# Kernel tuning notes

Hardware: AMD Instinct MI355X
Metric: run time of the kernel (lower is better)

## Reference

```python
import jax, jax.numpy as jnp
import numpy as np

N_CLAUSES = 200000
N_FEATURES = 64
HIDDEN = 128
N_STEPS = 512


def setup_inputs() -> dict:
    key = jax.random.key(0)
    ks = jax.random.split(key, 8)
    features = jax.random.normal(ks[0], (N_CLAUSES, N_FEATURES), jnp.float32)
    W1 = jax.random.normal(ks[1], (N_FEATURES, HIDDEN), jnp.float32) / np.sqrt(N_FEATURES)
    b1 = jnp.zeros((HIDDEN,), jnp.float32)
    W2 = jax.random.normal(ks[2], (HIDDEN, HIDDEN), jnp.float32) / np.sqrt(HIDDEN)
    b2 = jnp.zeros((HIDDEN,), jnp.float32)
    key_w = jax.random.normal(ks[3], (HIDDEN,), jnp.float32) / np.sqrt(HIDDEN)
    # sel_mask[s, n] = clause n is in the passive set at SEL step s
    sel_mask = jax.random.bernoulli(ks[4], 0.5, (N_STEPS, N_CLAUSES))
    # proof_mask[n] = clause n participates in the final proof (sparse)
    proof_mask = jax.random.bernoulli(ks[5], 0.02, (N_CLAUSES,))
    # guarantee passive & proof nonempty at every step (torch code divides by its size)
    proof_mask = proof_mask.at[0].set(True)
    sel_mask = sel_mask.at[:, 0].set(True)
    return {
        "features": features, "W1": W1, "b1": b1, "W2": W2, "b2": b2,
        "key_w": key_w, "sel_mask": sel_mask, "proof_mask": proof_mask,
    }


def reference(features, W1, b1, W2, b2, key_w, sel_mask, proof_mask):
    # clause_embedder: 2-layer MLP; clause_key: dot with key vector -> one logit per clause
    h = jax.nn.relu(features @ W1 + b1)          # [N, H]
    emb = h @ W2 + b2                            # [N, H]
    logits = emb @ key_w                         # [N]

    neg = jnp.finfo(logits.dtype).min
    masked = jnp.where(sel_mask, logits[None, :], neg)   # [S, N]
    lse = jax.nn.logsumexp(masked, axis=1)                # [S] log-softmax denominator over passive set

    tgt = sel_mask & proof_mask[None, :]                  # [S, N] passive & proof
    cnt = tgt.sum(axis=1).astype(logits.dtype)            # [S] (>=1 by construction)
    # soft-target CE: -sum_j t_j * log_softmax(logits)_j, t uniform over tgt
    num = jnp.where(tgt, logits[None, :], 0.0).sum(axis=1) / cnt
    loss = (lse - num).mean()                             # mean over SEL steps
    return loss
```

## Files before the change

kernel.cpp:

```cpp
#include <hip/hip_runtime.h>
#include <hip/hip_bf16.h>

#define DEV __device__ __forceinline__

constexpr int NC = 200000;
constexpr int NF = 64;
constexpr int NH = 128;
constexpr int NS = 512;

constexpr int OF_CFG   = 0;
constexpr int OF_W1    = 16;
constexpr int OF_B1    = OF_W1 + NF * NH;
constexpr int OF_W2K   = OF_B1 + NH;
constexpr int OF_B2K   = OF_W2K + NH;
constexpr int OF_MAX   = OF_B2K + 1;
constexpr int OF_ACCE  = OF_MAX + 1;
constexpr int OF_ACCP  = OF_ACCE + NS;
constexpr int OF_ACCC  = OF_ACCP + NS;
constexpr int OF_LOGIT = 16384;
constexpr int OF_E     = OF_LOGIT + NC;
constexpr int OF_PL    = OF_E + NC;
constexpr int OF_PC    = OF_PL + NC;

DEV float bf2f(unsigned short u) { return __uint_as_float(((unsigned)u) << 16); }

DEV float loadF(const void* p, int i, int fk) {
    return fk ? bf2f(((const unsigned short*)p)[i]) : ((const float*)p)[i];
}

DEV unsigned flipf(float x) {
    unsigned u = __float_as_uint(x);
    return (u & 0x80000000u) ? ~u : (u | 0x80000000u);
}
DEV float unflipf(unsigned u) {
    unsigned b = (u & 0x80000000u) ? (u ^ 0x80000000u) : ~u;
    return __uint_as_float(b);
}

DEV bool okhalf(unsigned h) { return h == 0u || h == 1u || h == 0x3F80u || h == 0x3C00u; }

__global__ void k_probe(const void* features, const void* W1, const void* b1,
                        const void* W2, const void* b2, const void* keyw,
                        const void* sel, float* ws) {
    __shared__ int s_tiny, s_w4, s_w2;
    __shared__ float kw[NH];
    __shared__ float pr[NH];
    int tx = threadIdx.x;
    if (tx == 0) { s_tiny = 0; s_w4 = 1; s_w2 = 1; }
    __syncthreads();
    {
        const unsigned short* u = (const unsigned short*)features;
        unsigned e = (u[tx] >> 7) & 0xFFu;
        if (e < 100u) atomicAdd(&s_tiny, 1);
        const unsigned* w = (const unsigned*)sel;
        unsigned v = w[tx];
        if (!(v == 0u || v == 1u || v == 0x3F800000u)) atomicAnd(&s_w4, 0);
        if (!(okhalf(v & 0xFFFFu) && okhalf(v >> 16))) atomicAnd(&s_w2, 0);
    }
    __syncthreads();
    int fk = (s_tiny >= 8) ? 0 : 1;
    int mw = s_w4 ? 4 : (s_w2 ? 2 : 1);
    if (tx == 0) { ((int*)ws)[0] = fk; ((int*)ws)[1] = mw; }
    if (tx < NH) kw[tx] = loadF(keyw, tx, fk);
    for (int i = tx; i < NF * NH; i += blockDim.x) {
        int f = i >> 7;
        int j = i & (NH - 1);
        int jc = j >> 2, c = j & 3;
        ws[OF_W1 + ((jc * NF + f) << 2) + c] = loadF(W1, i, fk);
    }
    if (tx < NH) ws[OF_B1 + tx] = loadF(b1, tx, fk);
    __syncthreads();
    if (tx < NH) {
        float s = 0.f;
        for (int k = 0; k < NH; k++) s += loadF(W2, tx * NH + k, fk) * kw[k];
        ws[OF_W2K + tx] = s;
        pr[tx] = loadF(b2, tx, fk) * kw[tx];
    }
    __syncthreads();
    if (tx == 0) {
        float s = 0.f;
        for (int k = 0; k < NH; k++) s += pr[k];
        ws[OF_B2K] = s;
        ((unsigned*)ws)[OF_MAX] = 0u;
    }
    for (int i = tx; i < 3 * NS; i += blockDim.x) ws[OF_ACCE + i] = 0.f;
}

__global__ __launch_bounds__(256) void k_logits(const void* features,
                                                const float* __restrict__ w1t,
                                                const float* __restrict__ bias1,
                                                const float* __restrict__ wk,
                                                const float* __restrict__ cfg,
                                                float* __restrict__ logits,
                                                unsigned* __restrict__ maxp) {
    __shared__ float sred[4];
    int tx = threadIdx.x;
    int fk = ((const int*)cfg)[0];
    float b2k = cfg[OF_B2K];
    int n = blockIdx.x * 256 + tx;
    float acc = -3.0e38f;
    if (n < NC) {
        float feat[NF];
        if (fk) {
            const uint4* fp = (const uint4*)((const unsigned short*)features + (size_t)n * NF);
            #pragma unroll
            for (int q = 0; q < 8; q++) {
                uint4 v = fp[q];
                unsigned vv[4] = {v.x, v.y, v.z, v.w};
                #pragma unroll
                for (int h = 0; h < 4; h++) {
                    feat[q * 8 + h * 2 + 0] = __uint_as_float(vv[h] << 16);
                    feat[q * 8 + h * 2 + 1] = __uint_as_float(vv[h] & 0xFFFF0000u);
                }
            }
        } else {
            const float4* fp = (const float4*)((const float*)features + (size_t)n * NF);
            #pragma unroll
            for (int q = 0; q < 16; q++) {
                float4 v = fp[q];
                feat[q * 4 + 0] = v.x; feat[q * 4 + 1] = v.y;
                feat[q * 4 + 2] = v.z; feat[q * 4 + 3] = v.w;
            }
        }
        acc = b2k;
        for (int jc = 0; jc < NH / 4; jc++) {
            const float4* wp = (const float4*)(w1t + (size_t)jc * (NF * 4));
            float4 b = *(const float4*)(bias1 + jc * 4);
            float d0 = b.x, d1 = b.y, d2 = b.z, d3 = b.w;
            #pragma unroll
            for (int f = 0; f < NF; f++) {
                float4 w = wp[f];
                d0 += feat[f] * w.x; d1 += feat[f] * w.y;
                d2 += feat[f] * w.z; d3 += feat[f] * w.w;
            }
            float4 k4 = *(const float4*)(wk + jc * 4);
            acc += fmaxf(d0, 0.f) * k4.x + fmaxf(d1, 0.f) * k4.y
                 + fmaxf(d2, 0.f) * k4.z + fmaxf(d3, 0.f) * k4.w;
        }
        logits[n] = acc;
    }
    float m = acc;
    #pragma unroll
    for (int k = 1; k < 64; k <<= 1) m = fmaxf(m, __shfl_xor(m, k, 64));
    if ((tx & 63) == 0) sred[tx >> 6] = m;
    __syncthreads();
    if (tx == 0) {
        m = fmaxf(fmaxf(sred[0], sred[1]), fmaxf(sred[2], sred[3]));
        atomicMax(maxp, flipf(m));
    }
}

__global__ void k_prep(const void* proof, float* ws) {
    int n = blockIdx.x * 256 + threadIdx.x;
    if (n >= NC) return;
    int mw = ((const int*)ws)[1];
    float M = unflipf(((const unsigned*)ws)[OF_MAX]);
    float l = ws[OF_LOGIT + n];
    ws[OF_E + n] = __expf(l - M);
    bool pf;
    if (mw == 1)      pf = ((const unsigned char*)proof)[n] != 0;
    else if (mw == 2) pf = ((const unsigned short*)proof)[n] != 0;
    else              pf = ((const unsigned*)proof)[n] != 0;
    ws[OF_PL + n] = pf ? l : 0.f;
    ws[OF_PC + n] = pf ? 1.f : 0.f;
}

constexpr int NT_N = 16;
constexpr int BL_N = 256 * NT_N;
constexpr int SG = 32;

template<int MW>
DEV void bloop(const void* sel, int s0, int baddr,
               const float (&e)[NT_N], const float (&pl)[NT_N], const float (&pc)[NT_N],
               float* ws) {
    for (int si = 0; si < SG; si++) {
        int s = s0 + si;
        size_t off = (size_t)s * NC + (size_t)baddr;
        float m[NT_N];
        if (MW == 1) {
            uint4 w = *(const uint4*)((const unsigned char*)sel + off);
            unsigned v[4] = {w.x, w.y, w.z, w.w};
            #pragma unroll
            for (int q = 0; q < 4; q++)
                #pragma unroll
                for (int b = 0; b < 4; b++)
                    m[q * 4 + b] = ((v[q] >> (8 * b)) & 0xFFu) ? 1.f : 0.f;
        } else if (MW == 2) {
            const uint4* p = (const uint4*)((const unsigned short*)sel + off);
            #pragma unroll
            for (int h = 0; h < 2; h++) {
                uint4 w = p[h];
                unsigned v[4] = {w.x, w.y, w.z, w.w};
                #pragma unroll
                for (int q = 0; q < 4; q++) {
                    m[h * 8 + q * 2 + 0] = (v[q] & 0xFFFFu) ? 1.f : 0.f;
                    m[h * 8 + q * 2 + 1] = (v[q] >> 16) ? 1.f : 0.f;
                }
            }
        } else {
            const uint4* p = (const uint4*)((const unsigned*)sel + off);
            #pragma unroll
            for (int q = 0; q < 4; q++) {
                uint4 w = p[q];
                m[q * 4 + 0] = w.x ? 1.f : 0.f; m[q * 4 + 1] = w.y ? 1.f : 0.f;
                m[q * 4 + 2] = w.z ? 1.f : 0.f; m[q * 4 + 3] = w.w ? 1.f : 0.f;
            }
        }
        float se = 0.f, sp = 0.f, sc = 0.f;
        #pragma unroll
        for (int i = 0; i < NT_N; i++) {
            se += m[i] * e[i]; sp += m[i] * pl[i]; sc += m[i] * pc[i];
        }
        #pragma unroll
        for (int k = 1; k < 64; k <<= 1) {
            se += __shfl_xor(se, k, 64);
            sp += __shfl_xor(sp, k, 64);
            sc += __shfl_xor(sc, k, 64);
        }
        if ((threadIdx.x & 63) == 0) {
            atomicAdd(&ws[OF_ACCE + s], se);
            atomicAdd(&ws[OF_ACCP + s], sp);
            atomicAdd(&ws[OF_ACCC + s], sc);
        }
    }
}

__global__ __launch_bounds__(256) void k_phaseB(const void* sel, float* ws) {
    int tx = threadIdx.x;
    int base = blockIdx.x * BL_N + tx * NT_N;
    int s0 = blockIdx.y * SG;
    bool active = base < NC;
    int baddr = active ? base : 0;
    float e[NT_N], pl[NT_N], pc[NT_N];
    #pragma unroll
    for (int q = 0; q < 4; q++) {
        float4 ve = active ? ((const float4*)&ws[OF_E + baddr])[q]  : make_float4(0, 0, 0, 0);
        float4 vp = active ? ((const float4*)&ws[OF_PL + baddr])[q] : make_float4(0, 0, 0, 0);
        float4 vc = active ? ((const float4*)&ws[OF_PC + baddr])[q] : make_float4(0, 0, 0, 0);
        e[q * 4 + 0] = ve.x; e[q * 4 + 1] = ve.y; e[q * 4 + 2] = ve.z; e[q * 4 + 3] = ve.w;
        pl[q * 4 + 0] = vp.x; pl[q * 4 + 1] = vp.y; pl[q * 4 + 2] = vp.z; pl[q * 4 + 3] = vp.w;
        pc[q * 4 + 0] = vc.x; pc[q * 4 + 1] = vc.y; pc[q * 4 + 2] = vc.z; pc[q * 4 + 3] = vc.w;
    }
    int mw = ((const int*)ws)[1];
    if (mw == 1)      bloop<1>(sel, s0, baddr, e, pl, pc, ws);
    else if (mw == 2) bloop<2>(sel, s0, baddr, e, pl, pc, ws);
    else              bloop<4>(sel, s0, baddr, e, pl, pc, ws);
}

__global__ void k_final(float* ws, void* out) {
    __shared__ float sred[256];
    int tx = threadIdx.x;
    float M = unflipf(((const unsigned*)ws)[OF_MAX]);
    float sum = 0.f;
    for (int s = tx; s < NS; s += 256) {
        float lse = M + logf(ws[OF_ACCE + s]);
        sum += lse - ws[OF_ACCP + s] / ws[OF_ACCC + s];
    }
    sred[tx] = sum;
    __syncthreads();
    for (int k = 128; k > 0; k >>= 1) {
        if (tx < k) sred[tx] += sred[tx + k];
        __syncthreads();
    }
    if (tx == 0) {
        float loss = sred[0] / (float)NS;
        int fk = ((const int*)ws)[0];
        if (fk) ((__hip_bfloat16*)out)[0] = __float2bfloat16(loss);
        else    ((float*)out)[0] = loss;
    }
}

extern "C" void kernel_launch(void* const* d_in, const int* in_sizes, int n_in,
                              void* d_out, int out_size, void* d_ws, size_t ws_size,
                              hipStream_t stream) {
    const void* features = d_in[0];
    const void* W1   = d_in[1];
    const void* b1   = d_in[2];
    const void* W2   = d_in[3];
    const void* b2   = d_in[4];
    const void* keyw = d_in[5];
    const void* sel  = d_in[6];
    const void* proof = d_in[7];
    float* ws = (float*)d_ws;

    k_probe<<<1, 256, 0, stream>>>(features, W1, b1, W2, b2, keyw, sel, ws);
    int nblk = (NC + 255) / 256;
    k_logits<<<nblk, 256, 0, stream>>>(features, ws + OF_W1, ws + OF_B1, ws + OF_W2K,
                                       ws, ws + OF_LOGIT, (unsigned*)ws + OF_MAX);
    k_prep<<<nblk, 256, 0, stream>>>(proof, ws);
    dim3 gB((NC + BL_N - 1) / BL_N, NS / SG);
    k_phaseB<<<gB, 256, 0, stream>>>(sel, ws);
    k_final<<<1, 256, 0, stream>>>(ws, d_out);
}
```

Measured before the change: 702.2 us.

## Compute clause logits with bf16 MFMA using split-precision hi/lo operands

Rewrites the first MLP layer of the logits kernel to use 16x16x32 bf16 MFMA instructions instead of per-thread scalar FMA loops. Weights are pre-swizzled into MFMA operand layout in the probe kernel, and fp32 inputs are split into bf16 high and low parts, using three MFMA products to approximate fp32 accuracy. Each wave handles 32 rows, and the logits reduction goes through cross-lane shuffles. This targets the compute-bound GEMM cost of the logits stage, at the cost of extra MFMAs and conversions and slightly different rounding.

```diff
diff --git a/kernel.cpp b/kernel.cpp
--- a/kernel.cpp
+++ b/kernel.cpp
@@ -9,23 +9,33 @@
 constexpr int NS = 512;
 
 constexpr int OF_CFG   = 0;
-constexpr int OF_W1    = 16;
-constexpr int OF_B1    = OF_W1 + NF * NH;
+constexpr int OF_B1    = 16;
 constexpr int OF_W2K   = OF_B1 + NH;
 constexpr int OF_B2K   = OF_W2K + NH;
 constexpr int OF_MAX   = OF_B2K + 1;
-constexpr int OF_ACCE  = OF_MAX + 1;
+constexpr int OF_ACCE  = 288;
 constexpr int OF_ACCP  = OF_ACCE + NS;
 constexpr int OF_ACCC  = OF_ACCP + NS;
+constexpr int OF_W1H   = 2048;
+constexpr int OF_W1L   = 6144;
 constexpr int OF_LOGIT = 16384;
 constexpr int OF_E     = OF_LOGIT + NC;
 constexpr int OF_PL    = OF_E + NC;
 constexpr int OF_PC    = OF_PL + NC;
 
+using short8  = __attribute__((ext_vector_type(8))) short;
+using floatx4 = __attribute__((ext_vector_type(4))) float;
+
 DEV float bf2f(unsigned short u) { return __uint_as_float(((unsigned)u) << 16); }
 
 DEV float loadF(const void* p, int i, int fk) {
     return fk ? bf2f(((const unsigned short*)p)[i]) : ((const float*)p)[i];
+}
+
+DEV unsigned short f2bf(float x) {
+    unsigned u = __float_as_uint(x);
+    unsigned r = ((u >> 16) & 1u) + 0x7FFFu;
+    return (unsigned short)((u + r) >> 16);
 }
 
 DEV unsigned flipf(float x) {
@@ -52,8 +62,8 @@
         const unsigned short* u = (const unsigned short*)features;
         unsigned e = (u[tx] >> 7) & 0xFFu;
         if (e < 100u) atomicAdd(&s_tiny, 1);
-        const unsigned* w = (const unsigned*)sel;
-        unsigned v = w[tx];
+        const unsigned* wrd = (const unsigned*)sel;
+        unsigned v = wrd[tx];
         if (!(v == 0u || v == 1u || v == 0x3F800000u)) atomicAnd(&s_w4, 0);
         if (!(okhalf(v & 0xFFFFu) && okhalf(v >> 16))) atomicAnd(&s_w2, 0);
     }
@@ -62,13 +72,26 @@
     int mw = s_w4 ? 4 : (s_w2 ? 2 : 1);
     if (tx == 0) { ((int*)ws)[0] = fk; ((int*)ws)[1] = mw; }
     if (tx < NH) kw[tx] = loadF(keyw, tx, fk);
+    if (tx < NH) ws[OF_B1 + tx] = loadF(b1, tx, fk);
+    unsigned short* w1h = (unsigned short*)(ws + OF_W1H);
+    unsigned short* w1l = (unsigned short*)(ws + OF_W1L);
     for (int i = tx; i < NF * NH; i += blockDim.x) {
-        int f = i >> 7;
-        int j = i & (NH - 1);
-        int jc = j >> 2, c = j & 3;
-        ws[OF_W1 + ((jc * NF + f) << 2) + c] = loadF(W1, i, fk);
-    }
-    if (tx < NH) ws[OF_B1 + tx] = loadF(b1, tx, fk);
+        int j    = i & 7;
+        int lane = (i >> 3) & 63;
+        int ks   = (i >> 9) & 1;
+        int c    = i >> 10;
+        int k    = ks * 32 + ((lane >> 4) << 3) + j;
+        int col  = c * 16 + (lane & 15);
+        if (fk) {
+            w1h[i] = ((const unsigned short*)W1)[k * NH + col];
+            w1l[i] = 0;
+        } else {
+            float x = ((const float*)W1)[k * NH + col];
+            unsigned short h = f2bf(x);
+            w1h[i] = h;
+            w1l[i] = f2bf(x - __uint_as_float(((unsigned)h) << 16));
+        }
+    }
     __syncthreads();
     if (tx < NH) {
         float s = 0.f;
@@ -86,63 +109,107 @@
     for (int i = tx; i < 3 * NS; i += blockDim.x) ws[OF_ACCE + i] = 0.f;
 }
 
-__global__ __launch_bounds__(256) void k_logits(const void* features,
-                                                const float* __restrict__ w1t,
-                                                const float* __restrict__ bias1,
-                                                const float* __restrict__ wk,
-                                                const float* __restrict__ cfg,
+__global__ __launch_bounds__(256) void k_logits(const void* __restrict__ features,
+                                                const float* __restrict__ ws,
                                                 float* __restrict__ logits,
                                                 unsigned* __restrict__ maxp) {
     __shared__ float sred[4];
-    int tx = threadIdx.x;
-    int fk = ((const int*)cfg)[0];
-    float b2k = cfg[OF_B2K];
-    int n = blockIdx.x * 256 + tx;
-    float acc = -3.0e38f;
-    if (n < NC) {
-        float feat[NF];
+    const int tx = threadIdx.x, w = tx >> 6, l = tx & 63;
+    const int fk = ((const int*)ws)[0];
+    const float b2k = ws[OF_B2K];
+    const int rbase = blockIdx.x * 128 + w * 32;
+    const int lrow = l & 15;
+    const int lk = (l >> 4) << 3;
+
+    short8 ah[2][2], al[2][2];
+    if (fk) {
+        const unsigned short* f = (const unsigned short*)features;
+        #pragma unroll
+        for (int rt = 0; rt < 2; rt++) {
+            int row = rbase + rt * 16 + lrow; if (row > NC - 1) row = NC - 1;
+            #pragma unroll
+            for (int ks = 0; ks < 2; ks++)
+                ah[rt][ks] = *(const short8*)(f + (size_t)row * NF + ks * 32 + lk);
+        }
+    } else {
+        const float* f = (const float*)features;
+        #pragma unroll
+        for (int rt = 0; rt < 2; rt++) {
+            int row = rbase + rt * 16 + lrow; if (row > NC - 1) row = NC - 1;
+            #pragma unroll
+            for (int ks = 0; ks < 2; ks++) {
+                const float* p = f + (size_t)row * NF + ks * 32 + lk;
+                float4 v0 = *(const float4*)p;
+                float4 v1 = *(const float4*)(p + 4);
+                float xs[8] = {v0.x, v0.y, v0.z, v0.w, v1.x, v1.y, v1.z, v1.w};
+                #pragma unroll
+                for (int j = 0; j < 8; j++) {
+                    unsigned short h = f2bf(xs[j]);
+                    ah[rt][ks][j] = (short)h;
+                    al[rt][ks][j] = (short)f2bf(xs[j] - __uint_as_float(((unsigned)h) << 16));
+                }
+            }
+        }
+    }
+
+    const short8* w1h = (const short8*)(ws + OF_W1H);
+    const short8* w1l = (const short8*)(ws + OF_W1L);
+    float pr[2][4] = {{0.f, 0.f, 0.f, 0.f}, {0.f, 0.f, 0.f, 0.f}};
+
+    #pragma unroll 2
+    for (int c = 0; c < 8; c++) {
+        short8 bh0 = w1h[(c * 2 + 0) * 64 + l];
+        short8 bh1 = w1h[(c * 2 + 1) * 64 + l];
+        float b1v = ws[OF_B1 + c * 16 + lrow];
+        float wkv = ws[OF_W2K + c * 16 + lrow];
         if (fk) {
-            const uint4* fp = (const uint4*)((const unsigned short*)features + (size_t)n * NF);
-            #pragma unroll
-            for (int q = 0; q < 8; q++) {
-                uint4 v = fp[q];
-                unsigned vv[4] = {v.x, v.y, v.z, v.w};
-                #pragma unroll
-                for (int h = 0; h < 4; h++) {
-                    feat[q * 8 + h * 2 + 0] = __uint_as_float(vv[h] << 16);
-                    feat[q * 8 + h * 2 + 1] = __uint_as_float(vv[h] & 0xFFFF0000u);
-                }
+            #pragma unroll
+            for (int rt = 0; rt < 2; rt++) {
+                floatx4 acc = {0.f, 0.f, 0.f, 0.f};
+                acc = __builtin_amdgcn_mfma_f32_16x16x32_bf16(ah[rt][0], bh0, acc, 0, 0, 0);
+                acc = __builtin_amdgcn_mfma_f32_16x16x32_bf16(ah[rt][1], bh1, acc, 0, 0, 0);
+                #pragma unroll
+                for (int r = 0; r < 4; r++) pr[rt][r] += fmaxf(acc[r] + b1v, 0.f) * wkv;
             }
         } else {
-            const float4* fp = (const float4*)((const float*)features + (size_t)n * NF);
-            #pragma unroll
-            for (int q = 0; q < 16; q++) {
-                float4 v = fp[q];
-                feat[q * 4 + 0] = v.x; feat[q * 4 + 1] = v.y;
-                feat[q * 4 + 2] = v.z; feat[q * 4 + 3] = v.w;
-            }
-        }
-        acc = b2k;
-        for (int jc = 0; jc < NH / 4; jc++) {
-            const float4* wp = (const float4*)(w1t + (size_t)jc * (NF * 4));
-            float4 b = *(const float4*)(bias1 + jc * 4);
-            float d0 = b.x, d1 = b.y, d2 = b.z, d3 = b.w;
-            #pragma unroll
-            for (int f = 0; f < NF; f++) {
-                float4 w = wp[f];
-                d0 += feat[f] * w.x; d1 += feat[f] * w.y;
-                d2 += feat[f] * w.z; d3 += feat[f] * w.w;
-            }
-            float4 k4 = *(const float4*)(wk + jc * 4);
-            acc += fmaxf(d0, 0.f) * k4.x + fmaxf(d1, 0.f) * k4.y
-                 + fmaxf(d2, 0.f) * k4.z + fmaxf(d3, 0.f) * k4.w;
-        }
-        logits[n] = acc;
-    }
-    float m = acc;
+            short8 bl0 = w1l[(c * 2 + 0) * 64 + l];
+            short8 bl1 = w1l[(c * 2 + 1) * 64 + l];
+            #pragma unroll
+            for (int rt = 0; rt < 2; rt++) {
+                floatx4 acc = {0.f, 0.f, 0.f, 0.f};
+                acc = __builtin_amdgcn_mfma_f32_16x16x32_bf16(ah[rt][0], bh0, acc, 0, 0, 0);
+                acc = __builtin_amdgcn_mfma_f32_16x16x32_bf16(ah[rt][1], bh1, acc, 0, 0, 0);
+                acc = __builtin_amdgcn_mfma_f32_16x16x32_bf16(ah[rt][0], bl0, acc, 0, 0, 0);
+                acc = __builtin_amdgcn_mfma_f32_16x16x32_bf16(ah[rt][1], bl1, acc, 0, 0, 0);
+                acc = __builtin_amdgcn_mfma_f32_16x16x32_bf16(al[rt][0], bh0, acc, 0, 0, 0);
+                acc = __builtin_amdgcn_mfma_f32_16x16x32_bf16(al[rt][1], bh1, acc, 0, 0, 0);
+                #pragma unroll
+                for (int r = 0; r < 4; r++) pr[rt][r] += fmaxf(acc[r] + b1v, 0.f) * wkv;
+            }
+        }
+    }
+
+    float m = -3.0e38f;
     #pragma unroll
-    for (int k = 1; k < 64; k <<= 1) m = fmaxf(m, __shfl_xor(m, k, 64));
-    if ((tx & 63) == 0) sred[tx >> 6] = m;
+    for (int rt = 0; rt < 2; rt++) {
+        #pragma unroll
+        for (int r = 0; r < 4; r++) {
+            float v = pr[rt][r];
+            v += __shfl_xor(v, 1, 64);
+            v += __shfl_xor(v, 2, 64);
+            v += __shfl_xor(v, 4, 64);
+            v += __shfl_xor(v, 8, 64);
+            v += b2k;
+            int row = rbase + rt * 16 + (l >> 4) * 4 + r;
+            if (row < NC) {
+                m = fmaxf(m, v);
+                if (lrow == 0) logits[row] = v;
+            }
+        }
+    }
+    m = fmaxf(m, __shfl_xor(m, 16, 64));
+    m = fmaxf(m, __shfl_xor(m, 32, 64));
+    if (l == 0) sred[w] = m;
     __syncthreads();
     if (tx == 0) {
         m = fmaxf(fmaxf(sred[0], sred[1]), fmaxf(sred[2], sred[3]));
@@ -284,9 +351,9 @@
     float* ws = (float*)d_ws;
 
     k_probe<<<1, 256, 0, stream>>>(features, W1, b1, W2, b2, keyw, sel, ws);
+    int nblkL = (NC + 127) / 128;
+    k_logits<<<nblkL, 256, 0, stream>>>(features, ws, ws + OF_LOGIT, (unsigned*)ws + OF_MAX);
     int nblk = (NC + 255) / 256;
-    k_logits<<<nblk, 256, 0, stream>>>(features, ws + OF_W1, ws + OF_B1, ws + OF_W2K,
-                                       ws, ws + OF_LOGIT, (unsigned*)ws + OF_MAX);
     k_prep<<<nblk, 256, 0, stream>>>(proof, ws);
     dim3 gB((NC + BL_N - 1) / BL_N, NS / SG);
     k_phaseB<<<gB, 256, 0, stream>>>(sel, ws);
```

Measured after the change: 671.2 us. 1.05x faster.
